# Kernel tuning notes

Measured on AMD Instinct MI355X. Metric: run time of the kernel, lower is better.

## Reference

```python
import jax, jax.numpy as jnp
import numpy as np

B, S, H = 32, 2048, 1024
A = 1024  # attention_hidden_size
EPS = 1e-5


def setup_inputs() -> dict:
    key = jax.random.key(0)
    ks = jax.random.split(key, 16)
    sc_h = 1.0 / np.sqrt(H)
    sc_a = 1.0 / np.sqrt(A)
    sc_2h = 1.0 / np.sqrt(2 * H)
    return {
        "seq_states": jax.random.normal(ks[0], (B, S, H), jnp.float32),
        "q_state": jax.random.normal(ks[1], (B, H), jnp.float32),
        "Wk": jax.random.uniform(ks[2], (H, A), jnp.float32, -sc_h, sc_h),
        "bk": jax.random.uniform(ks[3], (A,), jnp.float32, -sc_h, sc_h),
        "Wq": jax.random.uniform(ks[4], (H, A), jnp.float32, -sc_h, sc_h),
        "bq": jax.random.uniform(ks[5], (A,), jnp.float32, -sc_h, sc_h),
        "Wg": jax.random.uniform(ks[6], (A, A), jnp.float32, -sc_a, sc_a),
        "bg": jax.random.uniform(ks[7], (A,), jnp.float32, -sc_a, sc_a),
        "Ws": jax.random.uniform(ks[8], (A, 1), jnp.float32, -sc_a, sc_a),
        "bs": jax.random.uniform(ks[9], (1,), jnp.float32, -sc_a, sc_a),
        "Wo": jax.random.uniform(ks[10], (2 * H, H), jnp.float32, -sc_2h, sc_2h),
        "bo": jax.random.uniform(ks[11], (H,), jnp.float32, -sc_2h, sc_2h),
        "gamma": jnp.ones((H,), jnp.float32),
        "beta": jnp.zeros((H,), jnp.float32),
    }


def reference(seq_states, q_state, Wk, bk, Wq, bq, Wg, bg, Ws, bs, Wo, bo, gamma, beta):
    keys = jnp.einsum("bsh,ha->bsa", seq_states, Wk) + bk          # [B,S,A]
    query = (q_state @ Wq + bq)[:, None, :]                          # [B,1,A]
    alignment = jnp.tanh(keys + query)                               # [B,S,A]
    gate = jax.nn.sigmoid(jnp.einsum("bsa,ac->bsc", alignment, Wg) + bg)
    gated = alignment * gate                                         # dropout p=0.0 -> identity
    scores = jnp.einsum("bsa,ao->bso", gated, Ws)[..., 0] + bs[0]    # [B,S]
    weights = jax.nn.softmax(scores, axis=1)                         # [B,S]
    context = jnp.einsum("bs,bsh->bh", weights, seq_states)          # [B,H]
    fused_in = jnp.concatenate([context, q_state], axis=-1)          # [B,2H]
    pre = fused_in @ Wo + bo + q_state                               # residual
    mu = jnp.mean(pre, axis=-1, keepdims=True)
    var = jnp.var(pre, axis=-1, keepdims=True)
    fused = (pre - mu) * jax.lax.rsqrt(var + EPS) * gamma + beta
    return (fused, weights)
```

## Files before the change

kernel.cpp:

```cpp
#include <hip/hip_runtime.h>

typedef __attribute__((ext_vector_type(8))) short bf16x8;
typedef __attribute__((ext_vector_type(8))) unsigned short ushort8;
typedef __attribute__((ext_vector_type(4))) unsigned short ushortx4;
typedef __attribute__((ext_vector_type(4))) float f32x4;

#define BM 256
#define BN 256
#define BK 64

__device__ __forceinline__ unsigned short f2bf(float f) {
  union { float f; unsigned u; } c; c.f = f;
  return (unsigned short)((c.u + 0x7fffu + ((c.u >> 16) & 1u)) >> 16);
}
__device__ __forceinline__ float bf2f(unsigned short u) {
  union { unsigned u; float f; } c; c.u = ((unsigned)u) << 16;
  return c.f;
}
__device__ __forceinline__ float fast_tanh(float x) {
  float e = __expf(2.f * x);
  return 1.f - 2.f * __builtin_amdgcn_rcpf(e + 1.f);
}
__device__ __forceinline__ float fast_sigmoid(float x) {
  return __builtin_amdgcn_rcpf(1.f + __expf(-x));
}
__device__ __forceinline__ void gload16(const void* g, void* lds) {
  __builtin_amdgcn_global_load_lds(
      (const __attribute__((address_space(1))) unsigned int*)g,
      (__attribute__((address_space(3))) unsigned int*)lds, 16, 0, 0);
}
__device__ __forceinline__ void bar() {
  asm volatile("" ::: "memory");
  __builtin_amdgcn_s_barrier();
  asm volatile("" ::: "memory");
}
__device__ __forceinline__ void lgkm0_fence() {
  asm volatile("s_waitcnt lgkmcnt(0)" ::: "memory");
  __builtin_amdgcn_sched_barrier(0);
}
template <int N> __device__ __forceinline__ void vwait() {
  if constexpr (N < 0) {
  } else if constexpr (N == 2) asm volatile("s_waitcnt vmcnt(2)" ::: "memory");
  else if constexpr (N == 0) asm volatile("s_waitcnt vmcnt(0)" ::: "memory");
}

__device__ __forceinline__ void mfma16(const bf16x8 (&a)[4], const bf16x8 (&b)[4], int ro,
                                       f32x4 (&acc)[8][4]) {
  __builtin_amdgcn_s_setprio(1);
#pragma unroll
  for (int i = 0; i < 4; ++i)
#pragma unroll
    for (int n = 0; n < 4; ++n)
      acc[ro + i][n] =
          __builtin_amdgcn_mfma_f32_16x16x32_bf16(a[i], b[n], acc[ro + i][n], 0, 0, 0);
  __builtin_amdgcn_s_setprio(0);
}

template <bool ST, int W1, int W4>
__device__ __forceinline__ void ktile(
    const char* rAk0, const char* rAk1,
    const char* rBk0, const char* rBk1,
    char* dNA, char* dNB,
    const unsigned short* pA0, const unsigned short* pA1,
    const unsigned short* pB0, const unsigned short* pB1,
    int kN, f32x4 (&acc)[8][4]) {
  bf16x8 a[4], a2[4], b[4];
#pragma unroll
  for (int i = 0; i < 4; ++i) a[i] = *(const bf16x8*)(rAk0 + i * 2048);
#pragma unroll
  for (int n = 0; n < 4; ++n)
    b[n] = *(const bf16x8*)(rBk0 + (n >> 1) * 16384 + (n & 1) * 2048);
  if (ST) {
    gload16(pB0 + 32768 + kN, dNB + 16384);
    gload16(pB1 + 32768 + kN, dNB + 16384 + 8192);
  }
  vwait<W1>();
  bar();
  lgkm0_fence();
  mfma16(a, b, 0, acc);
  bar();
#pragma unroll
  for (int i = 0; i < 4; ++i) a2[i] = *(const bf16x8*)(rAk0 + 16384 + i * 2048);
  if (ST) {
    gload16(pA0 + kN, dNA);
    gload16(pA1 + kN, dNA + 8192);
  }
  bar();
  lgkm0_fence();
  mfma16(a2, b, 4, acc);
  bar();
#pragma unroll
  for (int i = 0; i < 4; ++i) a[i] = *(const bf16x8*)(rAk1 + i * 2048);
#pragma unroll
  for (int n = 0; n < 4; ++n)
    b[n] = *(const bf16x8*)(rBk1 + (n >> 1) * 16384 + (n & 1) * 2048);
  if (ST) {
    gload16(pB0 + kN, dNB);
    gload16(pB1 + kN, dNB + 8192);
  }
  bar();
  lgkm0_fence();
  mfma16(a, b, 0, acc);
  bar();
#pragma unroll
  for (int i = 0; i < 4; ++i) a2[i] = *(const bf16x8*)(rAk1 + 16384 + i * 2048);
  if (ST) {
    gload16(pA0 + 65536 + kN, dNA + 16384);
    gload16(pA1 + 65536 + kN, dNA + 16384 + 8192);
  }
  vwait<W4>();
  bar();
  lgkm0_fence();
  mfma16(a2, b, 4, acc);
  bar();
}

#define GEMM_SETUP_AND_PIPELINE(Ag, Bg)                                                    \
  int t = threadIdx.x, lane = t & 63, wave = t >> 6;                                       \
  int wr = wave >> 2, wc = wave & 3;                                                       \
  int sl0 = ((lane >> 4) ^ (lane & 7)) * 16;                                               \
  int sl1 = (((lane >> 4) + 4) ^ (lane & 7)) * 16;                                         \
  int aLane = (wr * 64 + (lane & 15)) * 128;                                               \
  int bLane = (wc * 32 + (lane & 15)) * 128;                                               \
  const char* rA0k0 = (const char*)As0 + aLane + sl0;                                      \
  const char* rA0k1 = (const char*)As0 + aLane + sl1;                                      \
  const char* rA1k0 = (const char*)As1 + aLane + sl0;                                      \
  const char* rA1k1 = (const char*)As1 + aLane + sl1;                                      \
  const char* rB0k0 = (const char*)Bs0 + bLane + sl0;                                      \
  const char* rB0k1 = (const char*)Bs0 + bLane + sl1;                                      \
  const char* rB1k0 = (const char*)Bs1 + bLane + sl0;                                      \
  const char* rB1k1 = (const char*)Bs1 + bLane + sl1;                                      \
  char* dA0 = (char*)As0 + t * 16;                                                         \
  char* dA1 = (char*)As1 + t * 16;                                                         \
  char* dB0 = (char*)Bs0 + t * 16;                                                         \
  char* dB1 = (char*)Bs1 + t * 16;                                                         \
  int l3 = t >> 3;                                                                         \
  int sgE = ((t & 7) ^ (l3 & 7)) * 8;                                                      \
  const unsigned short* pA0 = Ag + (size_t)(m0 + l3) * 1024 + sgE;                         \
  const unsigned short* pA1 = pA0 + (size_t)128 * 1024;                                    \
  int nB0 = ((l3 >> 5) << 6) + (l3 & 31);                                                  \
  const unsigned short* pB0 = Bg + (size_t)(n0 + nB0) * 1024 + sgE;                        \
  const unsigned short* pB1 = pB0 + (size_t)128 * 1024;                                    \
  f32x4 acc[8][4] = {};                                                                    \
             \
  gload16(pA0, dA0); gload16(pA1, dA0 + 8192);                                             \
  gload16(pB0, dB0); gload16(pB1, dB0 + 8192);                                             \
  gload16(pB0 + 32768, dB0 + 16384); gload16(pB1 + 32768, dB0 + 16384 + 8192);             \
  gload16(pA0 + 65536, dA0 + 16384); gload16(pA1 + 65536, dA0 + 16384 + 8192);             \
  vwait<2>();                                                                              \
  bar();                                                                                   \
  _Pragma("unroll 1") for (int kt = 0; kt < 14; kt += 2) {                                 \
    ktile<true, 2, 2>(rA0k0, rA0k1, rB0k0, rB0k1, dA1, dB1, pA0, pA1, pB0, pB1,            \
                      (kt + 1) * 64, acc);                                                 \
    ktile<true, 2, 2>(rA1k0, rA1k1, rB1k0, rB1k1, dA0, dB0, pA0, pA1, pB0, pB1,            \
                      (kt + 2) * 64, acc);                                                 \
  }                                                                                        \
  ktile<true, 2, 2>(rA0k0, rA0k1, rB0k0, rB0k1, dA1, dB1, pA0, pA1, pB0, pB1, 960, acc);   \
  ktile<false, 0, -1>(rA1k0, rA1k1, rB1k0, rB1k1, dA0, dB0, pA0, pA1, pB0, pB1, 0, acc);

__device__ __forceinline__ void tile_coords(int bid, int& m0, int& n0, int& nt) {
  int lin = (bid & 7) * 128 + (bid >> 3);
  int mt = lin >> 2;
  nt = lin & 3;
  m0 = mt * BM;
  n0 = nt * BN;
}

__global__ __launch_bounds__(256) void prep_kernel(
    const float* __restrict__ seq, unsigned short* __restrict__ seqb,
    const float* __restrict__ Wk, const float* __restrict__ Wg,
    unsigned short* __restrict__ WkT, unsigned short* __restrict__ WgT,
    const float* __restrict__ q, const float* __restrict__ Wq,
    float* __restrict__ qp) {
  __shared__ float smem[4160];
  int bid = blockIdx.x, t = threadIdx.x;
  if (bid < 2048) {
    size_t i = ((size_t)bid * 256 + t) * 8;
    const size_t stride = (size_t)2048 * 256 * 8;
    for (; i < (size_t)67108864; i += stride) {
      f32x4 v0 = *(const f32x4*)(seq + i);
      f32x4 v1 = *(const f32x4*)(seq + i + 4);
      ushort8 o;
#pragma unroll
      for (int k = 0; k < 4; ++k) { o[k] = f2bf(v0[k]); o[k + 4] = f2bf(v1[k]); }
      *(ushort8*)(seqb + i) = o;
    }
  } else if (bid < 2560) {
    int b2 = bid - 2048;
    int mat = b2 >> 8;
    int tid = b2 & 255;
    int tr = tid >> 4, tc = tid & 15;
    const float* src = mat ? Wg : Wk;
    unsigned short* dst = mat ? WgT : WkT;
    int r0 = tr * 64, c0 = tc * 64;
    int lr = t >> 6, lc = t & 63;
#pragma unroll
    for (int i = 0; i < 16; ++i) {
      int r = i * 4 + lr;
      smem[r * 65 + lc] = src[(size_t)(r0 + r) * 1024 + c0 + lc];
    }
    __syncthreads();
#pragma unroll
    for (int i = 0; i < 16; ++i) {
      int r = i * 4 + lr;
      dst[(size_t)(c0 + r) * 1024 + r0 + lc] = f2bf(smem[lc * 65 + r]);
    }
  } else {
    int b3 = bid - 2560;
    int ac = b3 & 3, hc = b3 >> 2;
    int h0 = hc * 128;
    for (int i = t; i < 4096; i += 256) {
      int b = i >> 7, hh = i & 127;
      smem[b * 128 + hh] = q[(size_t)b * 1024 + h0 + hh];
    }
    __syncthreads();
    int a = ac * 256 + t;
    float acc[32] = {};
    for (int hh = 0; hh < 128; hh += 4) {
      float w0 = Wq[(size_t)(h0 + hh) * 1024 + a];
      float w1 = Wq[(size_t)(h0 + hh + 1) * 1024 + a];
      float w2 = Wq[(size_t)(h0 + hh + 2) * 1024 + a];
      float w3 = Wq[(size_t)(h0 + hh + 3) * 1024 + a];
#pragma unroll
      for (int b = 0; b < 32; ++b) {
        f32x4 qv = *(const f32x4*)&smem[b * 128 + hh];
        acc[b] += qv[0] * w0 + qv[1] * w1 + qv[2] * w2 + qv[3] * w3;
      }
    }
#pragma unroll
    for (int b = 0; b < 32; ++b) qp[((size_t)(hc * 32 + b)) * 1024 + a] = acc[b];
  }
}

__global__ __launch_bounds__(512, 2) void gemm1_kernel(
    const unsigned short* __restrict__ seqb, const unsigned short* __restrict__ WkT,
    const float* __restrict__ qp, const float* __restrict__ bq,
    const float* __restrict__ bk, unsigned short* __restrict__ alignb) {
  __shared__ unsigned short As0[BM * BK], Bs0[BN * BK], As1[BM * BK], Bs1[BN * BK];
  int m0, n0, nt;
  tile_coords(blockIdx.x, m0, n0, nt);
  GEMM_SETUP_AND_PIPELINE(seqb, WkT)

  int bidx = m0 >> 11;
  float qv[4];
#pragma unroll
  for (int ni = 0; ni < 4; ++ni) {
    int col = n0 + wc * 64 + ni * 16 + (lane & 15);
    float s = bq[col] + bk[col];
#pragma unroll
    for (int hc = 0; hc < 8; ++hc) s += qp[((size_t)(hc * 32 + bidx)) * 1024 + col];
    qv[ni] = s;
  }
#pragma unroll
  for (int mi = 0; mi < 8; ++mi) {
    int row0 = m0 + wr * 128 + mi * 16 + ((lane >> 4) * 4);
#pragma unroll
    for (int ni = 0; ni < 4; ++ni) {
      int col = n0 + wc * 64 + ni * 16 + (lane & 15);
#pragma unroll
      for (int j = 0; j < 4; ++j) {
        float v = fast_tanh(acc[mi][ni][j] + qv[ni]);
        alignb[(size_t)(row0 + j) * 1024 + col] = f2bf(v);
      }
    }
  }
}

__global__ __launch_bounds__(512, 2) void gemm2_kernel(
    const unsigned short* __restrict__ alignb, const unsigned short* __restrict__ WgT,
    const float* __restrict__ bg, const float* __restrict__ Ws,
    float* __restrict__ scores_part) {
  __shared__ unsigned short As0[BM * BK], Bs0[BN * BK], As1[BM * BK], Bs1[BN * BK];
  __shared__ float sred[BM * 4];
  int m0, n0, nt;
  tile_coords(blockIdx.x, m0, n0, nt);
  GEMM_SETUP_AND_PIPELINE(alignb, WgT)

#pragma unroll
  for (int mi = 0; mi < 8; ++mi) {
#pragma unroll
    for (int j = 0; j < 4; ++j) {
      int rloc = wr * 128 + mi * 16 + ((lane >> 4) * 4) + j;
      int row = m0 + rloc;
      float p = 0.f;
#pragma unroll
      for (int ni = 0; ni < 4; ++ni) {
        int col = n0 + wc * 64 + ni * 16 + (lane & 15);
        float gate = fast_sigmoid(acc[mi][ni][j] + bg[col]);
        float al = bf2f(alignb[(size_t)row * 1024 + col]);
        p += al * gate * Ws[col];
      }
      p += __shfl_xor(p, 1);
      p += __shfl_xor(p, 2);
      p += __shfl_xor(p, 4);
      p += __shfl_xor(p, 8);
      if ((lane & 15) == 0) sred[rloc * 4 + wc] = p;
    }
  }
  __syncthreads();
  if (t < 256)
    scores_part[(size_t)nt * 65536 + m0 + t] =
        sred[t * 4] + sred[t * 4 + 1] + sred[t * 4 + 2] + sred[t * 4 + 3];
}

__global__ __launch_bounds__(256) void softmax_kernel(const float* __restrict__ sp,
                                                      float* __restrict__ wout) {
  __shared__ float red[256];
  int b = blockIdx.x, t = threadIdx.x;
  float sc[8];
  float lmax = -1e30f;
#pragma unroll
  for (int i = 0; i < 8; ++i) {
    int s = i * 256 + t;
    float v = 0.f;
#pragma unroll
    for (int n = 0; n < 4; ++n) v += sp[(size_t)n * 65536 + b * 2048 + s];
    sc[i] = v;
    lmax = fmaxf(lmax, v);
  }
  red[t] = lmax;
  __syncthreads();
  for (int off = 128; off > 0; off >>= 1) {
    if (t < off) red[t] = fmaxf(red[t], red[t + off]);
    __syncthreads();
  }
  float mx = red[0];
  __syncthreads();
  float lsum = 0.f;
#pragma unroll
  for (int i = 0; i < 8; ++i) {
    sc[i] = expf(sc[i] - mx);
    lsum += sc[i];
  }
  red[t] = lsum;
  __syncthreads();
  for (int off = 128; off > 0; off >>= 1) {
    if (t < off) red[t] += red[t + off];
    __syncthreads();
  }
  float inv = 1.f / red[0];
#pragma unroll
  for (int i = 0; i < 8; ++i) wout[(size_t)b * 2048 + i * 256 + t] = sc[i] * inv;
}

__global__ __launch_bounds__(256) void context_kernel(const unsigned short* __restrict__ seqb,
                                                      const float* __restrict__ wts,
                                                      float* __restrict__ ctx_part) {
  __shared__ float wsh[128];
  int b = blockIdx.x, t = threadIdx.x, s0 = blockIdx.z * 128;
  int h0 = t * 4;
  if (t < 128) wsh[t] = wts[(size_t)b * 2048 + s0 + t];
  __syncthreads();
  float a0 = 0.f, a1 = 0.f, a2 = 0.f, a3 = 0.f;
  const unsigned short* p = seqb + ((size_t)b * 2048 + s0) * 1024 + h0;
#pragma unroll 4
  for (int s = 0; s < 128; ++s) {
    ushortx4 v = *(const ushortx4*)(p + (size_t)s * 1024);
    float w = wsh[s];
    a0 += w * bf2f(v[0]);
    a1 += w * bf2f(v[1]);
    a2 += w * bf2f(v[2]);
    a3 += w * bf2f(v[3]);
  }
  float* dst = ctx_part + (size_t)(blockIdx.z * 32 + b) * 1024 + h0;
  dst[0] = a0; dst[1] = a1; dst[2] = a2; dst[3] = a3;
}

__global__ __launch_bounds__(256) void pre_kernel(const float* __restrict__ ctx_part,
                                                  const float* __restrict__ q,
                                                  const float* __restrict__ Wo,
                                                  float* __restrict__ pre_part) {
  __shared__ float fin[32 * 128];
  int kc = blockIdx.x, hc = blockIdx.y, t = threadIdx.x;
  int k0 = kc * 128, h0 = hc * 256;
  for (int i = t; i < 4096; i += 256) {
    int b = i >> 7, kk = i & 127, k = k0 + kk;
    float f;
    if (k < 1024) {
      f = 0.f;
#pragma unroll
      for (int s = 0; s < 16; ++s) f += ctx_part[((size_t)(s * 32 + b)) * 1024 + k];
    } else {
      f = q[(size_t)b * 1024 + (k - 1024)];
    }
    fin[b * 128 + kk] = f;
  }
  __syncthreads();
  int h = h0 + t;
  float acc[32] = {};
  for (int kk = 0; kk < 128; kk += 4) {
    float w0 = Wo[(size_t)(k0 + kk) * 1024 + h];
    float w1 = Wo[(size_t)(k0 + kk + 1) * 1024 + h];
    float w2 = Wo[(size_t)(k0 + kk + 2) * 1024 + h];
    float w3 = Wo[(size_t)(k0 + kk + 3) * 1024 + h];
#pragma unroll
    for (int b = 0; b < 32; ++b) {
      f32x4 fv = *(const f32x4*)&fin[b * 128 + kk];
      acc[b] += fv[0] * w0 + fv[1] * w1 + fv[2] * w2 + fv[3] * w3;
    }
  }
#pragma unroll
  for (int b = 0; b < 32; ++b) pre_part[((size_t)(kc * 32 + b)) * 1024 + h] = acc[b];
}

__global__ __launch_bounds__(256) void ln_kernel(const float* __restrict__ pre_part,
                                                 const float* __restrict__ q,
                                                 const float* __restrict__ bo,
                                                 const float* __restrict__ gamma,
                                                 const float* __restrict__ beta,
                                                 float* __restrict__ outF) {
  __shared__ float red[256];
  int b = blockIdx.x, t = threadIdx.x;
  float v[4];
  float lsum = 0.f;
#pragma unroll
  for (int i = 0; i < 4; ++i) {
    int h = i * 256 + t;
    float x = bo[h] + q[(size_t)b * 1024 + h];
#pragma unroll
    for (int kc = 0; kc < 16; ++kc) x += pre_part[((size_t)(kc * 32 + b)) * 1024 + h];
    v[i] = x;
    lsum += x;
  }
  red[t] = lsum;
  __syncthreads();
  for (int off = 128; off > 0; off >>= 1) {
    if (t < off) red[t] += red[t + off];
    __syncthreads();
  }
  float mu = red[0] * (1.f / 1024.f);
  __syncthreads();
  float lv = 0.f;
#pragma unroll
  for (int i = 0; i < 4; ++i) {
    float d = v[i] - mu;
    lv += d * d;
  }
  red[t] = lv;
  __syncthreads();
  for (int off = 128; off > 0; off >>= 1) {
    if (t < off) red[t] += red[t + off];
    __syncthreads();
  }
  float var = red[0] * (1.f / 1024.f);
  float rs = rsqrtf(var + 1e-5f);
#pragma unroll
  for (int i = 0; i < 4; ++i) {
    int h = i * 256 + t;
    outF[(size_t)b * 1024 + h] = (v[i] - mu) * rs * gamma[h] + beta[h];
  }
}

extern "C" void kernel_launch(void* const* d_in, const int* in_sizes, int n_in,
                              void* d_out, int out_size, void* d_ws, size_t ws_size,
                              hipStream_t stream) {
  const float* seq = (const float*)d_in[0];
  const float* q = (const float*)d_in[1];
  const float* Wk = (const float*)d_in[2];
  const float* bk = (const float*)d_in[3];
  const float* Wq = (const float*)d_in[4];
  const float* bq = (const float*)d_in[5];
  const float* Wg = (const float*)d_in[6];
  const float* bg = (const float*)d_in[7];
  const float* Ws = (const float*)d_in[8];
  const float* Wo = (const float*)d_in[10];
  const float* bo = (const float*)d_in[11];
  const float* gamma = (const float*)d_in[12];
  const float* beta = (const float*)d_in[13];

  float* outF = (float*)d_out;
  float* outW = outF + 32 * 1024;

  char* ws = (char*)d_ws;
  unsigned short* alignb = (unsigned short*)ws;  ws += (size_t)134217728;
  unsigned short* seqb = (unsigned short*)ws;    ws += (size_t)134217728;
  unsigned short* WkT = (unsigned short*)ws;     ws += 2097152;
  unsigned short* WgT = (unsigned short*)ws;     ws += 2097152;
  float* qp = (float*)ws;                        ws += 1048576;
  float* scores_part = (float*)ws;               ws += 1048576;
  float* ctx_part = (float*)ws;                  ws += 2097152;
  float* pre_part = (float*)ws;                  ws += 2097152;
  if (ws_size < (size_t)(ws - (char*)d_ws)) return;

  prep_kernel<<<2592, 256, 0, stream>>>(seq, seqb, Wk, Wg, WkT, WgT, q, Wq, qp);
  gemm1_kernel<<<1024, 512, 0, stream>>>(seqb, WkT, qp, bq, bk, alignb);
  gemm2_kernel<<<1024, 512, 0, stream>>>(alignb, WgT, bg, Ws, scores_part);
  softmax_kernel<<<32, 256, 0, stream>>>(scores_part, outW);
  context_kernel<<<dim3(32, 1, 16), 256, 0, stream>>>(seqb, outW, ctx_part);
  pre_kernel<<<dim3(16, 4), 256, 0, stream>>>(ctx_part, q, Wo, pre_part);
  ln_kernel<<<32, 256, 0, stream>>>(pre_part, q, bo, gamma, beta, outF);
}
```

Measured before the change: 509.5 us.

## Software-pipeline LDS fragment reads across MFMA phases with partial lgkmcnt waits

Restructures the bf16 GEMM k-tile loop so LDS fragment reads for the next MFMA phase are issued before the current MFMA batch. It waits with partial lgkmcnt counts instead of draining to zero, and cuts barriers from eight to about four per k-tile. The next tile's first A/B fragments are prefetched into persistent registers across ktile calls, and the global-to-LDS load order is rotated to match. This aims to hide LDS latency behind matrix-core work, at the cost of more live VGPRs and subtle hazards in the buffer reuse and wait counts.

```diff
diff --git a/kernel.cpp b/kernel.cpp
--- a/kernel.cpp
+++ b/kernel.cpp
@@ -34,9 +34,11 @@
   __builtin_amdgcn_s_barrier();
   asm volatile("" ::: "memory");
 }
-__device__ __forceinline__ void lgkm0_fence() {
-  asm volatile("s_waitcnt lgkmcnt(0)" ::: "memory");
-  __builtin_amdgcn_sched_barrier(0);
+__device__ __forceinline__ void sb0() { __builtin_amdgcn_sched_barrier(0); }
+template <int N> __device__ __forceinline__ void vlgkm() {
+  if constexpr (N == 0) asm volatile("s_waitcnt lgkmcnt(0)" ::: "memory");
+  else if constexpr (N == 4) asm volatile("s_waitcnt lgkmcnt(4)" ::: "memory");
+  else if constexpr (N == 8) asm volatile("s_waitcnt lgkmcnt(8)" ::: "memory");
 }
 template <int N> __device__ __forceinline__ void vwait() {
   if constexpr (N < 0) {
@@ -56,63 +58,52 @@
   __builtin_amdgcn_s_setprio(0);
 }
 
-template <bool ST, int W1, int W4>
+template <bool ST, bool ST4, bool RD4, int W3, int W4>
 __device__ __forceinline__ void ktile(
-    const char* rAk0, const char* rAk1,
-    const char* rBk0, const char* rBk1,
-    char* dNA, char* dNB,
+    const char* rAk0, const char* rAk1, const char* rBk1,
+    const char* rAk0n, const char* rBk0n,
+    char* dAn, char* dBn,
+    char* dAc,
     const unsigned short* pA0, const unsigned short* pA1,
     const unsigned short* pB0, const unsigned short* pB1,
-    int kN, f32x4 (&acc)[8][4]) {
-  bf16x8 a[4], a2[4], b[4];
-#pragma unroll
-  for (int i = 0; i < 4; ++i) a[i] = *(const bf16x8*)(rAk0 + i * 2048);
+    int kN1, int kN2,
+    bf16x8 (&aX)[4], bf16x8 (&aY)[4], bf16x8 (&b0)[4], bf16x8 (&b1)[4],
+    f32x4 (&acc)[8][4]) {
+  bar();
+#pragma unroll
+  for (int i = 0; i < 4; ++i) aY[i] = *(const bf16x8*)(rAk0 + 16384 + i * 2048);
+  if (ST) { gload16(pB0 + kN1, dBn); gload16(pB1 + kN1, dBn + 8192); }
+  vlgkm<4>(); sb0();
+  mfma16(aX, b0, 0, acc);
+  bar();
+#pragma unroll
+  for (int i = 0; i < 4; ++i) aX[i] = *(const bf16x8*)(rAk1 + i * 2048);
 #pragma unroll
   for (int n = 0; n < 4; ++n)
-    b[n] = *(const bf16x8*)(rBk0 + (n >> 1) * 16384 + (n & 1) * 2048);
-  if (ST) {
-    gload16(pB0 + 32768 + kN, dNB + 16384);
-    gload16(pB1 + 32768 + kN, dNB + 16384 + 8192);
-  }
-  vwait<W1>();
+    b1[n] = *(const bf16x8*)(rBk1 + (n >> 1) * 16384 + (n & 1) * 2048);
+  if (ST) { gload16(pB0 + 32768 + kN1, dBn + 16384); gload16(pB1 + 32768 + kN1, dBn + 16384 + 8192); }
+  vlgkm<8>(); sb0();
+  mfma16(aY, b0, 4, acc);
   bar();
-  lgkm0_fence();
-  mfma16(a, b, 0, acc);
+#pragma unroll
+  for (int i = 0; i < 4; ++i) aY[i] = *(const bf16x8*)(rAk1 + 16384 + i * 2048);
+  if (ST) { gload16(pA0 + 65536 + kN1, dAn + 16384); gload16(pA1 + 65536 + kN1, dAn + 16384 + 8192); }
+  vlgkm<4>(); sb0();
+  mfma16(aX, b1, 0, acc);
+  vwait<W3>();
   bar();
-#pragma unroll
-  for (int i = 0; i < 4; ++i) a2[i] = *(const bf16x8*)(rAk0 + 16384 + i * 2048);
-  if (ST) {
-    gload16(pA0 + kN, dNA);
-    gload16(pA1 + kN, dNA + 8192);
-  }
-  bar();
-  lgkm0_fence();
-  mfma16(a2, b, 4, acc);
-  bar();
-#pragma unroll
-  for (int i = 0; i < 4; ++i) a[i] = *(const bf16x8*)(rAk1 + i * 2048);
-#pragma unroll
-  for (int n = 0; n < 4; ++n)
-    b[n] = *(const bf16x8*)(rBk1 + (n >> 1) * 16384 + (n & 1) * 2048);
-  if (ST) {
-    gload16(pB0 + kN, dNB);
-    gload16(pB1 + kN, dNB + 8192);
-  }
-  bar();
-  lgkm0_fence();
-  mfma16(a, b, 0, acc);
-  bar();
-#pragma unroll
-  for (int i = 0; i < 4; ++i) a2[i] = *(const bf16x8*)(rAk1 + 16384 + i * 2048);
-  if (ST) {
-    gload16(pA0 + 65536 + kN, dNA + 16384);
-    gload16(pA1 + 65536 + kN, dNA + 16384 + 8192);
-  }
+  if (RD4) {
+#pragma unroll
+    for (int i = 0; i < 4; ++i) aX[i] = *(const bf16x8*)(rAk0n + i * 2048);
+#pragma unroll
+    for (int n = 0; n < 4; ++n)
+      b0[n] = *(const bf16x8*)(rBk0n + (n >> 1) * 16384 + (n & 1) * 2048);
+  }
+  if (ST4) { gload16(pA0 + kN2, dAc); gload16(pA1 + kN2, dAc + 8192); }
+  if (RD4) vlgkm<8>(); else vlgkm<0>();
+  sb0();
+  mfma16(aY, b1, 4, acc);
   vwait<W4>();
-  bar();
-  lgkm0_fence();
-  mfma16(a2, b, 4, acc);
-  bar();
 }
 
 #define GEMM_SETUP_AND_PIPELINE(Ag, Bg)                                                    \
@@ -142,21 +133,31 @@
   const unsigned short* pB0 = Bg + (size_t)(n0 + nB0) * 1024 + sgE;                        \
   const unsigned short* pB1 = pB0 + (size_t)128 * 1024;                                    \
   f32x4 acc[8][4] = {};                                                                    \
-             \
+  bf16x8 aX[4], aY[4], b0f[4], b1f[4];                                                     \
+                                         \
   gload16(pA0, dA0); gload16(pA1, dA0 + 8192);                                             \
   gload16(pB0, dB0); gload16(pB1, dB0 + 8192);                                             \
   gload16(pB0 + 32768, dB0 + 16384); gload16(pB1 + 32768, dB0 + 16384 + 8192);             \
   gload16(pA0 + 65536, dA0 + 16384); gload16(pA1 + 65536, dA0 + 16384 + 8192);             \
   vwait<2>();                                                                              \
   bar();                                                                                   \
+                             \
+  _Pragma("unroll") for (int i = 0; i < 4; ++i)                                            \
+      aX[i] = *(const bf16x8*)(rA0k0 + i * 2048);                                          \
+  _Pragma("unroll") for (int n = 0; n < 4; ++n)                                            \
+      b0f[n] = *(const bf16x8*)(rB0k0 + (n >> 1) * 16384 + (n & 1) * 2048);                \
+  gload16(pA0 + 64, dA1); gload16(pA1 + 64, dA1 + 8192);                                   \
+  vwait<2>();                                                                              \
   _Pragma("unroll 1") for (int kt = 0; kt < 14; kt += 2) {                                 \
-    ktile<true, 2, 2>(rA0k0, rA0k1, rB0k0, rB0k1, dA1, dB1, pA0, pA1, pB0, pB1,            \
-                      (kt + 1) * 64, acc);                                                 \
-    ktile<true, 2, 2>(rA1k0, rA1k1, rB1k0, rB1k1, dA0, dB0, pA0, pA1, pB0, pB1,            \
-                      (kt + 2) * 64, acc);                                                 \
+    ktile<true, true, true, 2, 2>(rA0k0, rA0k1, rB0k1, rA1k0, rB1k0, dA1, dB1, dA0,        \
+        pA0, pA1, pB0, pB1, (kt + 1) * 64, (kt + 2) * 64, aX, aY, b0f, b1f, acc);          \
+    ktile<true, true, true, 2, 2>(rA1k0, rA1k1, rB1k1, rA0k0, rB0k0, dA0, dB0, dA1,        \
+        pA0, pA1, pB0, pB1, (kt + 2) * 64, (kt + 3) * 64, aX, aY, b0f, b1f, acc);          \
   }                                                                                        \
-  ktile<true, 2, 2>(rA0k0, rA0k1, rB0k0, rB0k1, dA1, dB1, pA0, pA1, pB0, pB1, 960, acc);   \
-  ktile<false, 0, -1>(rA1k0, rA1k1, rB1k0, rB1k1, dA0, dB0, pA0, pA1, pB0, pB1, 0, acc);
+  ktile<true, false, true, 2, 0>(rA0k0, rA0k1, rB0k1, rA1k0, rB1k0, dA1, dB1, dA0,         \
+      pA0, pA1, pB0, pB1, 960, 0, aX, aY, b0f, b1f, acc);                                  \
+  ktile<false, false, false, -1, -1>(rA1k0, rA1k1, rB1k1, rA0k0, rB0k0, dA0, dB0, dA1,     \
+      pA0, pA1, pB0, pB1, 0, 0, aX, aY, b0f, b1f, acc);
 
 __device__ __forceinline__ void tile_coords(int bid, int& m0, int& n0, int& nt) {
   int lin = (bid & 7) * 128 + (bid >> 3);
```

Result: no change. 506.0 us (-0.7%).

## Replace 256x256 double-buffered GEMM pipeline with simple 128x128 single-buffer tiles

Applied to the files above, without the earlier changes.

Both large GEMM kernels move from a 256x256 tile, 512-thread, double-buffered, hand-scheduled pipeline to a 128x128 tile, 256-thread kernel. The new kernel uses a single LDS buffer and waits for all loads before computing each k-step. The grid grows to 4096 blocks, and the score partials grow to 8 column tiles, so softmax now sums 8 partials. This simplifies scheduling and raises occupancy, but gives up load/compute overlap and halves the data reuse per tile.

```diff
diff --git a/kernel.cpp b/kernel.cpp
--- a/kernel.cpp
+++ b/kernel.cpp
@@ -5,10 +5,6 @@
 typedef __attribute__((ext_vector_type(4))) unsigned short ushortx4;
 typedef __attribute__((ext_vector_type(4))) float f32x4;
 
-#define BM 256
-#define BN 256
-#define BK 64
-
 __device__ __forceinline__ unsigned short f2bf(float f) {
   union { float f; unsigned u; } c; c.f = f;
   return (unsigned short)((c.u + 0x7fffu + ((c.u >> 16) & 1u)) >> 16);
@@ -34,137 +30,62 @@
   __builtin_amdgcn_s_barrier();
   asm volatile("" ::: "memory");
 }
-__device__ __forceinline__ void lgkm0_fence() {
-  asm volatile("s_waitcnt lgkmcnt(0)" ::: "memory");
-  __builtin_amdgcn_sched_barrier(0);
-}
-template <int N> __device__ __forceinline__ void vwait() {
-  if constexpr (N < 0) {
-  } else if constexpr (N == 2) asm volatile("s_waitcnt vmcnt(2)" ::: "memory");
-  else if constexpr (N == 0) asm volatile("s_waitcnt vmcnt(0)" ::: "memory");
-}
-
-__device__ __forceinline__ void mfma16(const bf16x8 (&a)[4], const bf16x8 (&b)[4], int ro,
-                                       f32x4 (&acc)[8][4]) {
-  __builtin_amdgcn_s_setprio(1);
+__device__ __forceinline__ void vwait0() {
+  asm volatile("s_waitcnt vmcnt(0)" ::: "memory");
+}
+
+__device__ __forceinline__ void mfma16_4(const bf16x8 (&a)[4], const bf16x8 (&b)[4],
+                                         f32x4 (&acc)[4][4]) {
 #pragma unroll
   for (int i = 0; i < 4; ++i)
 #pragma unroll
     for (int n = 0; n < 4; ++n)
-      acc[ro + i][n] =
-          __builtin_amdgcn_mfma_f32_16x16x32_bf16(a[i], b[n], acc[ro + i][n], 0, 0, 0);
-  __builtin_amdgcn_s_setprio(0);
-}
-
-template <bool ST, int W1, int W4>
-__device__ __forceinline__ void ktile(
-    const char* rAk0, const char* rAk1,
-    const char* rBk0, const char* rBk1,
-    char* dNA, char* dNB,
-    const unsigned short* pA0, const unsigned short* pA1,
-    const unsigned short* pB0, const unsigned short* pB1,
-    int kN, f32x4 (&acc)[8][4]) {
-  bf16x8 a[4], a2[4], b[4];
-#pragma unroll
-  for (int i = 0; i < 4; ++i) a[i] = *(const bf16x8*)(rAk0 + i * 2048);
-#pragma unroll
-  for (int n = 0; n < 4; ++n)
-    b[n] = *(const bf16x8*)(rBk0 + (n >> 1) * 16384 + (n & 1) * 2048);
-  if (ST) {
-    gload16(pB0 + 32768 + kN, dNB + 16384);
-    gload16(pB1 + 32768 + kN, dNB + 16384 + 8192);
-  }
-  vwait<W1>();
-  bar();
-  lgkm0_fence();
-  mfma16(a, b, 0, acc);
-  bar();
-#pragma unroll
-  for (int i = 0; i < 4; ++i) a2[i] = *(const bf16x8*)(rAk0 + 16384 + i * 2048);
-  if (ST) {
-    gload16(pA0 + kN, dNA);
-    gload16(pA1 + kN, dNA + 8192);
-  }
-  bar();
-  lgkm0_fence();
-  mfma16(a2, b, 4, acc);
-  bar();
-#pragma unroll
-  for (int i = 0; i < 4; ++i) a[i] = *(const bf16x8*)(rAk1 + i * 2048);
-#pragma unroll
-  for (int n = 0; n < 4; ++n)
-    b[n] = *(const bf16x8*)(rBk1 + (n >> 1) * 16384 + (n & 1) * 2048);
-  if (ST) {
-    gload16(pB0 + kN, dNB);
-    gload16(pB1 + kN, dNB + 8192);
-  }
-  bar();
-  lgkm0_fence();
-  mfma16(a, b, 0, acc);
-  bar();
-#pragma unroll
-  for (int i = 0; i < 4; ++i) a2[i] = *(const bf16x8*)(rAk1 + 16384 + i * 2048);
-  if (ST) {
-    gload16(pA0 + 65536 + kN, dNA + 16384);
-    gload16(pA1 + 65536 + kN, dNA + 16384 + 8192);
-  }
-  vwait<W4>();
-  bar();
-  lgkm0_fence();
-  mfma16(a2, b, 4, acc);
-  bar();
-}
-
-#define GEMM_SETUP_AND_PIPELINE(Ag, Bg)                                                    \
-  int t = threadIdx.x, lane = t & 63, wave = t >> 6;                                       \
-  int wr = wave >> 2, wc = wave & 3;                                                       \
-  int sl0 = ((lane >> 4) ^ (lane & 7)) * 16;                                               \
-  int sl1 = (((lane >> 4) + 4) ^ (lane & 7)) * 16;                                         \
-  int aLane = (wr * 64 + (lane & 15)) * 128;                                               \
-  int bLane = (wc * 32 + (lane & 15)) * 128;                                               \
-  const char* rA0k0 = (const char*)As0 + aLane + sl0;                                      \
-  const char* rA0k1 = (const char*)As0 + aLane + sl1;                                      \
-  const char* rA1k0 = (const char*)As1 + aLane + sl0;                                      \
-  const char* rA1k1 = (const char*)As1 + aLane + sl1;                                      \
-  const char* rB0k0 = (const char*)Bs0 + bLane + sl0;                                      \
-  const char* rB0k1 = (const char*)Bs0 + bLane + sl1;                                      \
-  const char* rB1k0 = (const char*)Bs1 + bLane + sl0;                                      \
-  const char* rB1k1 = (const char*)Bs1 + bLane + sl1;                                      \
-  char* dA0 = (char*)As0 + t * 16;                                                         \
-  char* dA1 = (char*)As1 + t * 16;                                                         \
-  char* dB0 = (char*)Bs0 + t * 16;                                                         \
-  char* dB1 = (char*)Bs1 + t * 16;                                                         \
-  int l3 = t >> 3;                                                                         \
-  int sgE = ((t & 7) ^ (l3 & 7)) * 8;                                                      \
-  const unsigned short* pA0 = Ag + (size_t)(m0 + l3) * 1024 + sgE;                         \
-  const unsigned short* pA1 = pA0 + (size_t)128 * 1024;                                    \
-  int nB0 = ((l3 >> 5) << 6) + (l3 & 31);                                                  \
-  const unsigned short* pB0 = Bg + (size_t)(n0 + nB0) * 1024 + sgE;                        \
-  const unsigned short* pB1 = pB0 + (size_t)128 * 1024;                                    \
-  f32x4 acc[8][4] = {};                                                                    \
-             \
-  gload16(pA0, dA0); gload16(pA1, dA0 + 8192);                                             \
-  gload16(pB0, dB0); gload16(pB1, dB0 + 8192);                                             \
-  gload16(pB0 + 32768, dB0 + 16384); gload16(pB1 + 32768, dB0 + 16384 + 8192);             \
-  gload16(pA0 + 65536, dA0 + 16384); gload16(pA1 + 65536, dA0 + 16384 + 8192);             \
-  vwait<2>();                                                                              \
-  bar();                                                                                   \
-  _Pragma("unroll 1") for (int kt = 0; kt < 14; kt += 2) {                                 \
-    ktile<true, 2, 2>(rA0k0, rA0k1, rB0k0, rB0k1, dA1, dB1, pA0, pA1, pB0, pB1,            \
-                      (kt + 1) * 64, acc);                                                 \
-    ktile<true, 2, 2>(rA1k0, rA1k1, rB1k0, rB1k1, dA0, dB0, pA0, pA1, pB0, pB1,            \
-                      (kt + 2) * 64, acc);                                                 \
-  }                                                                                        \
-  ktile<true, 2, 2>(rA0k0, rA0k1, rB0k0, rB0k1, dA1, dB1, pA0, pA1, pB0, pB1, 960, acc);   \
-  ktile<false, 0, -1>(rA1k0, rA1k1, rB1k0, rB1k1, dA0, dB0, pA0, pA1, pB0, pB1, 0, acc);
-
-__device__ __forceinline__ void tile_coords(int bid, int& m0, int& n0, int& nt) {
-  int lin = (bid & 7) * 128 + (bid >> 3);
-  int mt = lin >> 2;
-  nt = lin & 3;
-  m0 = mt * BM;
-  n0 = nt * BN;
-}
+      acc[i][n] =
+          __builtin_amdgcn_mfma_f32_16x16x32_bf16(a[i], b[n], acc[i][n], 0, 0, 0);
+}
+
+#define GEMM128_SETUP(Ag, Bg)                                                            \
+  int lin = (blockIdx.x & 7) * 512 + (blockIdx.x >> 3);                                  \
+  int mt = lin >> 3, nt = lin & 7;                                                       \
+  int m0 = mt * 128, n0 = nt * 128;                                                      \
+  int t = threadIdx.x, lane = t & 63, wave = t >> 6;                                     \
+  int wr = wave >> 1, wc = wave & 1;                                                     \
+  int sl0 = ((lane >> 4) ^ (lane & 7)) * 16;                                             \
+  int sl1 = (((lane >> 4) + 4) ^ (lane & 7)) * 16;                                       \
+  const char* rAk0 = (const char*)As + (wr * 64 + (lane & 15)) * 128 + sl0;              \
+  const char* rAk1 = (const char*)As + (wr * 64 + (lane & 15)) * 128 + sl1;              \
+  const char* rBk0 = (const char*)Bs + (wc * 64 + (lane & 15)) * 128 + sl0;              \
+  const char* rBk1 = (const char*)Bs + (wc * 64 + (lane & 15)) * 128 + sl1;              \
+  int l3 = t >> 3;                                                                       \
+  int sgE = ((t & 7) ^ (l3 & 7)) * 8;                                                    \
+  const unsigned short* pA = Ag + (size_t)(m0 + l3) * 1024 + sgE;                        \
+  const unsigned short* pB = Bg + (size_t)(n0 + l3) * 1024 + sgE;                        \
+  char* dA = (char*)As + t * 16;                                                         \
+  char* dB = (char*)Bs + t * 16;                                                         \
+  f32x4 acc[4][4] = {};                                                                  \
+  _Pragma("unroll 1") for (int kt = 0; kt < 16; ++kt) {                                  \
+    int k0 = kt * 64;                                                                    \
+    _Pragma("unroll") for (int r = 0; r < 4; ++r) {                                      \
+      gload16(pA + (size_t)(r * 32) * 1024 + k0, dA + r * 4096);                         \
+      gload16(pB + (size_t)(r * 32) * 1024 + k0, dB + r * 4096);                         \
+    }                                                                                    \
+    vwait0();                                                                            \
+    bar();                                                                               \
+    {                                                                                    \
+      bf16x8 a[4], b[4];                                                                 \
+      _Pragma("unroll") for (int i = 0; i < 4; ++i)                                      \
+          a[i] = *(const bf16x8*)(rAk0 + i * 2048);                                      \
+      _Pragma("unroll") for (int n = 0; n < 4; ++n)                                      \
+          b[n] = *(const bf16x8*)(rBk0 + n * 2048);                                      \
+      mfma16_4(a, b, acc);                                                               \
+      _Pragma("unroll") for (int i = 0; i < 4; ++i)                                      \
+          a[i] = *(const bf16x8*)(rAk1 + i * 2048);                                      \
+      _Pragma("unroll") for (int n = 0; n < 4; ++n)                                      \
+          b[n] = *(const bf16x8*)(rBk1 + n * 2048);                                      \
+      mfma16_4(a, b, acc);                                                               \
+    }                                                                                    \
+    bar();                                                                               \
+  }
 
 __global__ __launch_bounds__(256) void prep_kernel(
     const float* __restrict__ seq, unsigned short* __restrict__ seqb,
@@ -232,14 +153,13 @@
   }
 }
 
-__global__ __launch_bounds__(512, 2) void gemm1_kernel(
+__global__ __launch_bounds__(256, 2) void gemm1_kernel(
     const unsigned short* __restrict__ seqb, const unsigned short* __restrict__ WkT,
     const float* __restrict__ qp, const float* __restrict__ bq,
     const float* __restrict__ bk, unsigned short* __restrict__ alignb) {
-  __shared__ unsigned short As0[BM * BK], Bs0[BN * BK], As1[BM * BK], Bs1[BN * BK];
-  int m0, n0, nt;
-  tile_coords(blockIdx.x, m0, n0, nt);
-  GEMM_SETUP_AND_PIPELINE(seqb, WkT)
+  __shared__ unsigned short As[128 * 64];
+  __shared__ unsigned short Bs[128 * 64];
+  GEMM128_SETUP(seqb, WkT)
 
   int bidx = m0 >> 11;
   float qv[4];
@@ -252,8 +172,8 @@
     qv[ni] = s;
   }
 #pragma unroll
-  for (int mi = 0; mi < 8; ++mi) {
-    int row0 = m0 + wr * 128 + mi * 16 + ((lane >> 4) * 4);
+  for (int mi = 0; mi < 4; ++mi) {
+    int row0 = m0 + wr * 64 + mi * 16 + ((lane >> 4) * 4);
 #pragma unroll
     for (int ni = 0; ni < 4; ++ni) {
       int col = n0 + wc * 64 + ni * 16 + (lane & 15);
@@ -266,21 +186,20 @@
   }
 }
 
-__global__ __launch_bounds__(512, 2) void gemm2_kernel(
+__global__ __launch_bounds__(256, 2) void gemm2_kernel(
     const unsigned short* __restrict__ alignb, const unsigned short* __restrict__ WgT,
     const float* __restrict__ bg, const float* __restrict__ Ws,
     float* __restrict__ scores_part) {
-  __shared__ unsigned short As0[BM * BK], Bs0[BN * BK], As1[BM * BK], Bs1[BN * BK];
-  __shared__ float sred[BM * 4];
-  int m0, n0, nt;
-  tile_coords(blockIdx.x, m0, n0, nt);
-  GEMM_SETUP_AND_PIPELINE(alignb, WgT)
-
-#pragma unroll
-  for (int mi = 0; mi < 8; ++mi) {
+  __shared__ unsigned short As[128 * 64];
+  __shared__ unsigned short Bs[128 * 64];
+  __shared__ float sred[128 * 2];
+  GEMM128_SETUP(alignb, WgT)
+
+#pragma unroll
+  for (int mi = 0; mi < 4; ++mi) {
 #pragma unroll
     for (int j = 0; j < 4; ++j) {
-      int rloc = wr * 128 + mi * 16 + ((lane >> 4) * 4) + j;
+      int rloc = wr * 64 + mi * 16 + ((lane >> 4) * 4) + j;
       int row = m0 + rloc;
       float p = 0.f;
 #pragma unroll
@@ -294,13 +213,11 @@
       p += __shfl_xor(p, 2);
       p += __shfl_xor(p, 4);
       p += __shfl_xor(p, 8);
-      if ((lane & 15) == 0) sred[rloc * 4 + wc] = p;
-    }
-  }
-  __syncthreads();
-  if (t < 256)
-    scores_part[(size_t)nt * 65536 + m0 + t] =
-        sred[t * 4] + sred[t * 4 + 1] + sred[t * 4 + 2] + sred[t * 4 + 3];
+      if ((lane & 15) == 0) sred[rloc * 2 + wc] = p;
+    }
+  }
+  __syncthreads();
+  if (t < 128) scores_part[(size_t)nt * 65536 + m0 + t] = sred[t * 2] + sred[t * 2 + 1];
 }
 
 __global__ __launch_bounds__(256) void softmax_kernel(const float* __restrict__ sp,
@@ -314,7 +231,7 @@
     int s = i * 256 + t;
     float v = 0.f;
 #pragma unroll
-    for (int n = 0; n < 4; ++n) v += sp[(size_t)n * 65536 + b * 2048 + s];
+    for (int n = 0; n < 8; ++n) v += sp[(size_t)n * 65536 + b * 2048 + s];
     sc[i] = v;
     lmax = fmaxf(lmax, v);
   }
@@ -477,14 +394,14 @@
   unsigned short* WkT = (unsigned short*)ws;     ws += 2097152;
   unsigned short* WgT = (unsigned short*)ws;     ws += 2097152;
   float* qp = (float*)ws;                        ws += 1048576;
-  float* scores_part = (float*)ws;               ws += 1048576;
+  float* scores_part = (float*)ws;               ws += 2097152;
   float* ctx_part = (float*)ws;                  ws += 2097152;
   float* pre_part = (float*)ws;                  ws += 2097152;
   if (ws_size < (size_t)(ws - (char*)d_ws)) return;
 
   prep_kernel<<<2592, 256, 0, stream>>>(seq, seqb, Wk, Wg, WkT, WgT, q, Wq, qp);
-  gemm1_kernel<<<1024, 512, 0, stream>>>(seqb, WkT, qp, bq, bk, alignb);
-  gemm2_kernel<<<1024, 512, 0, stream>>>(alignb, WgT, bg, Ws, scores_part);
+  gemm1_kernel<<<4096, 256, 0, stream>>>(seqb, WkT, qp, bq, bk, alignb);
+  gemm2_kernel<<<4096, 256, 0, stream>>>(alignb, WgT, bg, Ws, scores_part);
   softmax_kernel<<<32, 256, 0, stream>>>(scores_part, outW);
   context_kernel<<<dim3(32, 1, 16), 256, 0, stream>>>(seqb, outW, ctx_part);
   pre_kernel<<<dim3(16, 4), 256, 0, stream>>>(ctx_part, q, Wo, pre_part);
```

Measured after the change: 483.3 us. 5.1% less time.
